# Kernel tuning notes

Hardware: AMD Instinct MI355X
Metric: run time of the kernel (lower is better)

The kernel has to match this reference:

```python
import jax, jax.numpy as jnp
import numpy as np

# Fuzzy-logic decoder: rules = [[0,0,0],[1,0,1]] (hardcoded in the torch module's __init__).
# For each rule [p, a, b] firing on predicate p:
#   num[s,o] = max_k min(t[a, s, k], t[b, k, o])   (max-min relation composition)
# amalgamate(x, y) = x + y - x*y (probabilistic OR); new starts at 0, and
# amalgamate(x, 0) = x, so with exactly one rule per predicate:
#   t_new[p] = amalgamate(t[p], num_p) = t[p] + num_p - t[p]*num_p

def _compose(A, B):
    # A: [S, K], B: [K, O] -> max over k of elementwise min -> [S, O]
    return jnp.max(jnp.minimum(A[:, :, None], B[None, :, :]), axis=1)


def setup_inputs() -> dict:
    key = jax.random.key(0)
    t = jax.random.uniform(key, (2, 512, 512), dtype=jnp.float32)
    return {"t": t}


def reference(t) -> jnp.ndarray:
    t0, t1 = t[0], t[1]
    num0 = _compose(t0, t0)          # rule [0,0,0]
    num1 = _compose(t0, t1)          # rule [1,0,1]
    num = jnp.stack([num0, num1], axis=0)  # [2, S, O]
    return t + num - t * num         # amalgamate(t, num)
```

## Files before the change

### kernel.cpp

```cpp
#include <hip/hip_runtime.h>


#define SDIM 512
#define TS 64
#define TO 32
#define BK 64
#define BK2 32
#define NCH (SDIM / BK)
#define ASTR 36

typedef _Float16 h2 __attribute__((ext_vector_type(2)));

__device__ __forceinline__ h2 pack2(float a, float b) {
    return __builtin_bit_cast(h2, __builtin_amdgcn_cvt_pkrtz(a, b));
}
__device__ __forceinline__ h2 pmin(h2 a, h2 b) { return __builtin_elementwise_min(a, b); }
__device__ __forceinline__ h2 pmax(h2 a, h2 b) { return __builtin_elementwise_max(a, b); }

__global__ __launch_bounds__(256) void fuzzy_compose_kernel(
        const float* __restrict__ t, float* __restrict__ out) {
    __shared__ h2 Als[TS][ASTR];
    __shared__ h2 Bls[BK2][TO];

    const int tid = threadIdx.x;
    const int o0 = blockIdx.x * TO;
    const int s0 = blockIdx.y * TS;
    const int p  = blockIdx.z;

    const float* __restrict__ A = t;
    const float* __restrict__ B = t + p * (SDIM * SDIM);

    const int og = tid & 15, sg = tid >> 4;
    const int ol = og * 2, sl = sg * 4;

    const int ar = tid >> 2, aq = tid & 3;
    const int bk = tid >> 3, bq = tid & 7;

    const float4* __restrict__ Arow =
        reinterpret_cast<const float4*>(A + (s0 + ar) * SDIM);

    h2 acc[4][2];
    #pragma unroll
    for (int j = 0; j < 4; ++j)
        #pragma unroll
        for (int i = 0; i < 2; ++i)
            acc[j][i] = pack2(0.f, 0.f);

    float4 fa[4], fx, fy;
    #pragma unroll
    for (int q4 = 0; q4 < 4; ++q4) fa[q4] = Arow[aq * 4 + q4];
    fx = *reinterpret_cast<const float4*>(B + (2 * bk) * SDIM + o0 + bq * 4);
    fy = *reinterpret_cast<const float4*>(B + (2 * bk + 1) * SDIM + o0 + bq * 4);

    for (int c = 0; c < NCH; ++c) {
        #pragma unroll
        for (int q4 = 0; q4 < 4; ++q4) {
            Als[ar][aq * 8 + q4 * 2 + 0] = pack2(fa[q4].x, fa[q4].y);
            Als[ar][aq * 8 + q4 * 2 + 1] = pack2(fa[q4].z, fa[q4].w);
        }
        Bls[bk][bq * 4 + 0] = pack2(fx.x, fy.x);
        Bls[bk][bq * 4 + 1] = pack2(fx.y, fy.y);
        Bls[bk][bq * 4 + 2] = pack2(fx.z, fy.z);
        Bls[bk][bq * 4 + 3] = pack2(fx.w, fy.w);
        __syncthreads();

        if (c + 1 < NCH) {
            const int k0 = (c + 1) * BK;
            #pragma unroll
            for (int q4 = 0; q4 < 4; ++q4) fa[q4] = Arow[k0 / 4 + aq * 4 + q4];
            fx = *reinterpret_cast<const float4*>(B + (k0 + 2 * bk) * SDIM + o0 + bq * 4);
            fy = *reinterpret_cast<const float4*>(B + (k0 + 2 * bk + 1) * SDIM + o0 + bq * 4);
        }

        #pragma unroll
        for (int k2 = 0; k2 < BK2; ++k2) {
            const h2 b0 = Bls[k2][ol];
            const h2 b1 = Bls[k2][ol + 1];
            #pragma unroll
            for (int j = 0; j < 4; ++j) {
                const h2 a = Als[sl + j][k2];
                acc[j][0] = pmax(acc[j][0], pmin(a, b0));
                acc[j][1] = pmax(acc[j][1], pmin(a, b1));
            }
        }
        __syncthreads();
    }

    const float* __restrict__ tp = t + p * (SDIM * SDIM);
    float* __restrict__ op = out + p * (SDIM * SDIM);
    #pragma unroll
    for (int j = 0; j < 4; ++j) {
        const int row = s0 + sl + j;
        const float2 tv = *reinterpret_cast<const float2*>(tp + row * SDIM + o0 + ol);
        const float n0 = fmaxf((float)acc[j][0][0], (float)acc[j][0][1]);
        const float n1 = fmaxf((float)acc[j][1][0], (float)acc[j][1][1]);
        float2 r;
        r.x = tv.x + n0 - tv.x * n0;
        r.y = tv.y + n1 - tv.y * n1;
        *reinterpret_cast<float2*>(op + row * SDIM + o0 + ol) = r;
    }
}

extern "C" void kernel_launch(void* const* d_in, const int* in_sizes, int n_in,
                              void* d_out, int out_size, void* d_ws, size_t ws_size,
                              hipStream_t stream) {
    const float* t = (const float*)d_in[0];
    float* out = (float*)d_out;
    dim3 grid(SDIM / TO, SDIM / TS, 2);
    fuzzy_compose_kernel<<<grid, 256, 0, stream>>>(t, out);
}
```

Measured before the change: 72.22 us.

## Rewrite compose kernel in fp32 with wave-uniform scalar A rows and transposed B tile

Replaces the packed-fp16 max-min kernel with an fp32 version. Each wave owns four output rows whose A values are wave-uniform and can be read through scalar loads. Only B is staged in LDS, transposed so each lane reads a float4 of k values for its own output column. This removes the fp16 conversion and precision loss and drops A from LDS, but gives up 2-wide packed math and lowers per-thread output reuse from 8 to 4 elements.

```diff
diff --git a/kernel.cpp b/kernel.cpp
--- a/kernel.cpp
+++ b/kernel.cpp
@@ -2,102 +2,89 @@
 
 
 #define SDIM 512
-#define TS 64
-#define TO 32
 #define BK 64
-#define BK2 32
-#define NCH (SDIM / BK)
-#define ASTR 36
+#define NCH 8
+#define BKP 68
 
-typedef _Float16 h2 __attribute__((ext_vector_type(2)));
-
-__device__ __forceinline__ h2 pack2(float a, float b) {
-    return __builtin_bit_cast(h2, __builtin_amdgcn_cvt_pkrtz(a, b));
-}
-__device__ __forceinline__ h2 pmin(h2 a, h2 b) { return __builtin_elementwise_min(a, b); }
-__device__ __forceinline__ h2 pmax(h2 a, h2 b) { return __builtin_elementwise_max(a, b); }
-
-__global__ __launch_bounds__(256) void fuzzy_compose_kernel(
+__global__ __launch_bounds__(256, 2) void fuzzy_compose_kernel(
         const float* __restrict__ t, float* __restrict__ out) {
-    __shared__ h2 Als[TS][ASTR];
-    __shared__ h2 Bls[BK2][TO];
+    __shared__ float Bt[64][BKP];
 
     const int tid = threadIdx.x;
-    const int o0 = blockIdx.x * TO;
-    const int s0 = blockIdx.y * TS;
+    const int o0 = blockIdx.x * 64;
+    const int s0 = blockIdx.y * 16;
     const int p  = blockIdx.z;
+    const float* __restrict__ Bm = t + p * (SDIM * SDIM);
 
-    const float* __restrict__ A = t;
-    const float* __restrict__ B = t + p * (SDIM * SDIM);
+    const int lane = tid & 63;
+    const int wv = __builtin_amdgcn_readfirstlane(tid >> 6);
+    const int srow = s0 + wv * 4;
+    const float* __restrict__ A0 = t + (srow + 0) * SDIM;
+    const float* __restrict__ A1 = t + (srow + 1) * SDIM;
+    const float* __restrict__ A2 = t + (srow + 2) * SDIM;
+    const float* __restrict__ A3 = t + (srow + 3) * SDIM;
 
-    const int og = tid & 15, sg = tid >> 4;
-    const int ol = og * 2, sl = sg * 4;
+    const int kq = tid >> 4;
+    const int oq = tid & 15;
 
-    const int ar = tid >> 2, aq = tid & 3;
-    const int bk = tid >> 3, bq = tid & 7;
+    float fbuf[4][4];
+    #pragma unroll
+    for (int r = 0; r < 4; ++r)
+        *reinterpret_cast<float4*>(&fbuf[r][0]) =
+            *reinterpret_cast<const float4*>(Bm + (4 * kq + r) * SDIM + o0 + 4 * oq);
 
-    const float4* __restrict__ Arow =
-        reinterpret_cast<const float4*>(A + (s0 + ar) * SDIM);
-
-    h2 acc[4][2];
-    #pragma unroll
-    for (int j = 0; j < 4; ++j)
-        #pragma unroll
-        for (int i = 0; i < 2; ++i)
-            acc[j][i] = pack2(0.f, 0.f);
-
-    float4 fa[4], fx, fy;
-    #pragma unroll
-    for (int q4 = 0; q4 < 4; ++q4) fa[q4] = Arow[aq * 4 + q4];
-    fx = *reinterpret_cast<const float4*>(B + (2 * bk) * SDIM + o0 + bq * 4);
-    fy = *reinterpret_cast<const float4*>(B + (2 * bk + 1) * SDIM + o0 + bq * 4);
+    float acc0 = 0.f, acc1 = 0.f, acc2 = 0.f, acc3 = 0.f;
 
     for (int c = 0; c < NCH; ++c) {
         #pragma unroll
-        for (int q4 = 0; q4 < 4; ++q4) {
-            Als[ar][aq * 8 + q4 * 2 + 0] = pack2(fa[q4].x, fa[q4].y);
-            Als[ar][aq * 8 + q4 * 2 + 1] = pack2(fa[q4].z, fa[q4].w);
+        for (int j = 0; j < 4; ++j) {
+            float4 ty;
+            ty.x = fbuf[0][j]; ty.y = fbuf[1][j]; ty.z = fbuf[2][j]; ty.w = fbuf[3][j];
+            *reinterpret_cast<float4*>(&Bt[4 * oq + j][4 * kq]) = ty;
         }
-        Bls[bk][bq * 4 + 0] = pack2(fx.x, fy.x);
-        Bls[bk][bq * 4 + 1] = pack2(fx.y, fy.y);
-        Bls[bk][bq * 4 + 2] = pack2(fx.z, fy.z);
-        Bls[bk][bq * 4 + 3] = pack2(fx.w, fy.w);
         __syncthreads();
 
         if (c + 1 < NCH) {
-            const int k0 = (c + 1) * BK;
             #pragma unroll
-            for (int q4 = 0; q4 < 4; ++q4) fa[q4] = Arow[k0 / 4 + aq * 4 + q4];
-            fx = *reinterpret_cast<const float4*>(B + (k0 + 2 * bk) * SDIM + o0 + bq * 4);
-            fy = *reinterpret_cast<const float4*>(B + (k0 + 2 * bk + 1) * SDIM + o0 + bq * 4);
+            for (int r = 0; r < 4; ++r)
+                *reinterpret_cast<float4*>(&fbuf[r][0]) =
+                    *reinterpret_cast<const float4*>(
+                        Bm + ((c + 1) * BK + 4 * kq + r) * SDIM + o0 + 4 * oq);
         }
 
+        const float* __restrict__ a0 = A0 + c * BK;
+        const float* __restrict__ a1 = A1 + c * BK;
+        const float* __restrict__ a2 = A2 + c * BK;
+        const float* __restrict__ a3 = A3 + c * BK;
         #pragma unroll
-        for (int k2 = 0; k2 < BK2; ++k2) {
-            const h2 b0 = Bls[k2][ol];
-            const h2 b1 = Bls[k2][ol + 1];
+        for (int m = 0; m < 16; ++m) {
+            const float4 b = *reinterpret_cast<const float4*>(&Bt[lane][4 * m]);
+            const float bb[4] = {b.x, b.y, b.z, b.w};
             #pragma unroll
-            for (int j = 0; j < 4; ++j) {
-                const h2 a = Als[sl + j][k2];
-                acc[j][0] = pmax(acc[j][0], pmin(a, b0));
-                acc[j][1] = pmax(acc[j][1], pmin(a, b1));
+            for (int i = 0; i < 4; ++i) {
+                const int kk = 4 * m + i;
+                acc0 = fmaxf(acc0, fminf(a0[kk], bb[i]));
+                acc1 = fmaxf(acc1, fminf(a1[kk], bb[i]));
+                acc2 = fmaxf(acc2, fminf(a2[kk], bb[i]));
+                acc3 = fmaxf(acc3, fminf(a3[kk], bb[i]));
             }
         }
         __syncthreads();
     }
 
-    const float* __restrict__ tp = t + p * (SDIM * SDIM);
+    const float* __restrict__ tpp = t + p * (SDIM * SDIM);
     float* __restrict__ op = out + p * (SDIM * SDIM);
-    #pragma unroll
-    for (int j = 0; j < 4; ++j) {
-        const int row = s0 + sl + j;
-        const float2 tv = *reinterpret_cast<const float2*>(tp + row * SDIM + o0 + ol);
-        const float n0 = fmaxf((float)acc[j][0][0], (float)acc[j][0][1]);
-        const float n1 = fmaxf((float)acc[j][1][0], (float)acc[j][1][1]);
-        float2 r;
-        r.x = tv.x + n0 - tv.x * n0;
-        r.y = tv.y + n1 - tv.y * n1;
-        *reinterpret_cast<float2*>(op + row * SDIM + o0 + ol) = r;
+    {
+        const int col = o0 + lane;
+        float tv;
+        tv = tpp[(srow + 0) * SDIM + col];
+        op[(srow + 0) * SDIM + col] = tv + acc0 - tv * acc0;
+        tv = tpp[(srow + 1) * SDIM + col];
+        op[(srow + 1) * SDIM + col] = tv + acc1 - tv * acc1;
+        tv = tpp[(srow + 2) * SDIM + col];
+        op[(srow + 2) * SDIM + col] = tv + acc2 - tv * acc2;
+        tv = tpp[(srow + 3) * SDIM + col];
+        op[(srow + 3) * SDIM + col] = tv + acc3 - tv * acc3;
     }
 }
 
@@ -106,6 +93,6 @@
                               hipStream_t stream) {
     const float* t = (const float*)d_in[0];
     float* out = (float*)d_out;
-    dim3 grid(SDIM / TO, SDIM / TS, 2);
+    dim3 grid(8, 32, 2);
     fuzzy_compose_kernel<<<grid, 256, 0, stream>>>(t, out);
 }
```

Measured after the change: 83.51 us. +15.6%, slower.
